# Kernel optimization log

Measured on AMD Instinct MI355X. Metric: run time of the kernel, lower is better.

Reference implementation:

```python
import jax, jax.numpy as jnp
import numpy as np

EMB = 768
HEADS = 12


def setup_inputs() -> dict:
    key = jax.random.key(0)
    ks = jax.random.split(key, 5)
    B, N, E = 8, 1024, EMB
    x = jax.random.normal(ks[0], (B, N, E), dtype=jnp.float32)
    s = 1.0 / np.sqrt(E)
    W_qkv = jax.random.normal(ks[1], (E, 3 * E), dtype=jnp.float32) * s
    b_qkv = jnp.zeros((3 * E,), dtype=jnp.float32)
    W_fc = jax.random.normal(ks[2], (E, E), dtype=jnp.float32) * s
    b_fc = jnp.zeros((E,), dtype=jnp.float32)
    return {"x": x, "W_qkv": W_qkv, "b_qkv": b_qkv, "W_fc": W_fc, "b_fc": b_fc}


def reference(x, W_qkv, b_qkv, W_fc, b_fc):
    B, N, E = x.shape
    H = HEADS
    D = E // H
    qkv = x @ W_qkv + b_qkv                      # [B, N, 3E]
    q, k, v = jnp.split(qkv, 3, axis=-1)
    # b n (h d) -> b h n d
    def to_heads(t):
        return t.reshape(B, N, H, D).transpose(0, 2, 1, 3)
    q, k, v = to_heads(q), to_heads(k), to_heads(v)
    scale = 1.0 / jnp.sqrt(jnp.float32(E))       # NOTE: scales by sqrt(emb_size), not head dim
    attn = jnp.einsum('bhid,bhjd->bhij', q, k) * scale
    attn = jax.nn.softmax(attn, axis=-1)
    out = jnp.einsum('bhij,bhjd->bhid', attn, v)
    out = out.transpose(0, 2, 1, 3).reshape(B, N, E)  # b h n d -> b n (h d)
    return out @ W_fc + b_fc
```

## Files before the change

kernel.cpp:

```cpp
#include <hip/hip_runtime.h>


typedef unsigned short u16;
typedef unsigned int u32;
typedef __attribute__((ext_vector_type(8))) short short8;
typedef __attribute__((ext_vector_type(4))) float f32x4;

#define DEV static __device__ __forceinline__

DEV u16 f2bf(float f) {
  union { float f; u32 u; } v; v.f = f;
  return (u16)((v.u + 0x7FFFu + ((v.u >> 16) & 1u)) >> 16);
}

DEV void gload_lds16(const void* g, void* l) {
  __builtin_amdgcn_global_load_lds(
      (const __attribute__((address_space(1))) void*)g,
      (__attribute__((address_space(3))) void*)l, 16, 0, 0);
}

__global__ void cvt_bf16_kernel(const float* __restrict__ in, u16* __restrict__ out, int n8) {
  int idx = blockIdx.x * blockDim.x + threadIdx.x;
  int stride = gridDim.x * blockDim.x;
  for (int i = idx; i < n8; i += stride) {
    float4 a = reinterpret_cast<const float4*>(in)[2 * i];
    float4 b = reinterpret_cast<const float4*>(in)[2 * i + 1];
    uint4 o;
    o.x = f2bf(a.x) | ((u32)f2bf(a.y) << 16);
    o.y = f2bf(a.z) | ((u32)f2bf(a.w) << 16);
    o.z = f2bf(b.x) | ((u32)f2bf(b.y) << 16);
    o.w = f2bf(b.z) | ((u32)f2bf(b.w) << 16);
    reinterpret_cast<uint4*>(out)[i] = o;
  }
}

__global__ void trcvt_kernel(const float* __restrict__ in, u16* __restrict__ out,
                             int K, int Nn) {
  __shared__ u16 tile[64][72];
  int ntiles = Nn >> 6;
  int tk = blockIdx.x / ntiles, tn = blockIdx.x % ntiles;
  int k0 = tk << 6, n0 = tn << 6;
  int t = threadIdx.x;
  int r = t >> 4;
  int c4 = (t & 15) << 2;
#pragma unroll
  for (int ps = 0; ps < 4; ++ps) {
    int k = r + ps * 16;
    float4 v = *reinterpret_cast<const float4*>(&in[(size_t)(k0 + k) * Nn + n0 + c4]);
    tile[c4 + 0][k] = f2bf(v.x);
    tile[c4 + 1][k] = f2bf(v.y);
    tile[c4 + 2][k] = f2bf(v.z);
    tile[c4 + 3][k] = f2bf(v.w);
  }
  __syncthreads();
  int nr = t >> 3;
  int c8 = (t & 7) << 3;
#pragma unroll
  for (int ps = 0; ps < 2; ++ps) {
    int n = nr + ps * 32;
    uint4 v = *reinterpret_cast<const uint4*>(&tile[n][c8]);
    *reinterpret_cast<uint4*>(&out[(size_t)(n0 + n) * K + k0 + c8]) = v;
  }
}

__global__ void trv_kernel(const u16* __restrict__ vh, u16* __restrict__ vt) {
  __shared__ u16 tile[64][72];
  int nt = blockIdx.x & 15;
  int bh = blockIdx.x >> 4;
  int n0 = nt << 6;
  int t = threadIdx.x;
  int nr = t >> 3;
  int d8 = (t & 7) << 3;
  const u16* src = vh + ((size_t)bh * 1024 + n0) * 64;
#pragma unroll
  for (int ps = 0; ps < 2; ++ps) {
    int n = nr + ps * 32;
    uint4 v = *reinterpret_cast<const uint4*>(&src[(size_t)n * 64 + d8]);
    const u16* e = reinterpret_cast<const u16*>(&v);
#pragma unroll
    for (int j = 0; j < 8; ++j) tile[d8 + j][n] = e[j];
  }
  __syncthreads();
  u16* dst = vt + ((size_t)bh * 64) * 1024 + n0;
#pragma unroll
  for (int ps = 0; ps < 2; ++ps) {
    int d = nr + ps * 32;
    uint4 v = *reinterpret_cast<const uint4*>(&tile[d][d8]);
    *reinterpret_cast<uint4*>(&dst[(size_t)d * 1024 + d8]) = v;
  }
}

template <int MODE>
__global__ __launch_bounds__(256, 4) void gemm_bt(
    const u16* __restrict__ A, const u16* __restrict__ Bt,
    const float* __restrict__ bias, void* __restrict__ Cout,
    u16* __restrict__ qh, u16* __restrict__ kh, u16* __restrict__ vh,
    int Nn) {
  __shared__ u16 As[2][128 * 32];
  __shared__ u16 Bs[2][128 * 32];
  const int nTn = Nn >> 7;
  const int nwg = gridDim.x;
  int wg = blockIdx.x;
  wg = (wg & 7) * (nwg >> 3) + (wg >> 3);
  const int tm = wg / nTn, tn = wg % nTn;
  const int m0 = tm << 7, n0 = tn << 7;
  const int tid = threadIdx.x;
  const int w = tid >> 6, lane = tid & 63;
  const int g = lane >> 4, p = lane & 15;
  const int wr = w >> 1, wc = w & 1;

  const int srow = lane >> 2;
  const int schunk = (lane & 3) ^ ((srow >> 1) & 3);
  const u16* Asrc = A + (size_t)(m0 + srow) * 768 + schunk * 8;
  const u16* Bsrc = Bt + (size_t)(n0 + srow) * 768 + schunk * 8;
  const int csw = (g ^ ((p >> 1) & 3)) << 3;

  f32x4 acc[4][4] = {};

#define STAGE(kt, sbuf)                                                         \
  do {                                                                          \
    _Pragma("unroll")                                                           \
    for (int i = 0; i < 2; ++i) {                                               \
      int trow = w * 32 + i * 16;                                               \
      gload_lds16(Asrc + (size_t)trow * 768 + (kt) * 32, &As[sbuf][trow * 32]); \
      gload_lds16(Bsrc + (size_t)trow * 768 + (kt) * 32, &Bs[sbuf][trow * 32]); \
    }                                                                           \
  } while (0)

  STAGE(0, 0);
  __syncthreads();

  int buf = 0;
  for (int k = 0; k < 24; ++k) {
    const u16* as = As[buf];
    const u16* bs = Bs[buf];
    short8 af[4], bf[4];
#pragma unroll
    for (int mb = 0; mb < 4; ++mb)
      af[mb] = *reinterpret_cast<const short8*>(&as[(wr * 64 + mb * 16 + p) * 32 + csw]);
#pragma unroll
    for (int nb = 0; nb < 4; ++nb)
      bf[nb] = *reinterpret_cast<const short8*>(&bs[(wc * 64 + nb * 16 + p) * 32 + csw]);
    if (k < 23) STAGE(k + 1, buf ^ 1);
#pragma unroll
    for (int mb = 0; mb < 4; ++mb)
#pragma unroll
      for (int nb = 0; nb < 4; ++nb)
        acc[mb][nb] = __builtin_amdgcn_mfma_f32_16x16x32_bf16(af[mb], bf[nb], acc[mb][nb], 0, 0, 0);
    __syncthreads();
    buf ^= 1;
  }
#undef STAGE

  const float qscale = 0.036084391824351615f;
#pragma unroll
  for (int nb = 0; nb < 4; ++nb) {
    int ncol = n0 + wc * 64 + nb * 16 + p;
    float bv = bias[ncol];
    if (MODE == 0) {
#pragma unroll
      for (int mb = 0; mb < 4; ++mb)
#pragma unroll
        for (int r = 0; r < 4; ++r) {
          int m = m0 + wr * 64 + mb * 16 + g * 4 + r;
          ((float*)Cout)[(size_t)m * Nn + ncol] = acc[mb][nb][r] + bv;
        }
    } else {
      int h64 = ncol >> 6;
      int which = h64 / 12;
      int hh = h64 - which * 12;
      int d = ncol & 63;
      u16* dst = which == 0 ? qh : (which == 1 ? kh : vh);
      float sc = which == 0 ? qscale : 1.f;
#pragma unroll
      for (int mb = 0; mb < 4; ++mb)
#pragma unroll
        for (int r = 0; r < 4; ++r) {
          int m = m0 + wr * 64 + mb * 16 + g * 4 + r;
          int bb = m >> 10, nr = m & 1023;
          dst[(((size_t)bb * 12 + hh) * 1024 + nr) * 64 + d] = f2bf((acc[mb][nb][r] + bv) * sc);
        }
    }
  }
}

__global__ __launch_bounds__(512, 6) void attn_kernel(
    const u16* __restrict__ qh, const u16* __restrict__ kh,
    const u16* __restrict__ vt, u16* __restrict__ ao) {
  __shared__ u16 Ks[2][64 * 64];
  __shared__ u16 Vs[2][64 * 64];
  __shared__ u16 Ps[8][16 * 64];
  const int bid = blockIdx.x;
  const int qt = bid & 7;
  const int bh = bid >> 3;
  const int b = bh / 12, h = bh % 12;
  const int tid = threadIdx.x;
  const int w = tid >> 6, lane = tid & 63;
  const int g = lane >> 4, p = lane & 15;
  const int qrow = qt * 128 + w * 16;

  const u16* qbase = qh + ((size_t)bh * 1024 + qrow + p) * 64;
  short8 qf0 = *reinterpret_cast<const short8*>(qbase + g * 8);
  short8 qf1 = *reinterpret_cast<const short8*>(qbase + 32 + g * 8);

  const int ci = w * 64 + lane;
  const int crow = ci >> 3;
  const int csw = (ci & 7) ^ (crow & 7);
  const u16* ksrc = kh + (((size_t)bh * 1024 + crow) << 6) + csw * 8;
  const u16* vsrc = vt + ((size_t)bh * 64 + crow) * 1024 + csw * 8;
  u16* myp = Ps[w];

  const int sw = p & 7;
  const int c0 = (g ^ sw) << 3;
  const int c1 = ((4 + g) ^ sw) << 3;

  float m_run = -1e30f, l_run = 0.f;
  f32x4 oacc[4] = {};

  gload_lds16(ksrc, &Ks[0][w * 512]);
  gload_lds16(vsrc, &Vs[0][w * 512]);
  __syncthreads();

  int buf = 0;
  for (int kt = 0; kt < 1024; kt += 64) {
    if (kt < 960) {
      gload_lds16(ksrc + ((kt + 64) << 6), &Ks[buf ^ 1][w * 512]);
      gload_lds16(vsrc + (kt + 64), &Vs[buf ^ 1][w * 512]);
    }

    f32x4 s[4];
    __builtin_amdgcn_s_setprio(1);
#pragma unroll
    for (int jb = 0; jb < 4; ++jb) {
      const u16* kb = &Ks[buf][(jb * 16 + p) * 64];
      short8 k0 = *reinterpret_cast<const short8*>(kb + c0);
      short8 k1 = *reinterpret_cast<const short8*>(kb + c1);
      f32x4 z = {};
      z = __builtin_amdgcn_mfma_f32_16x16x32_bf16(k0, qf0, z, 0, 0, 0);
      z = __builtin_amdgcn_mfma_f32_16x16x32_bf16(k1, qf1, z, 0, 0, 0);
      s[jb] = z;
    }
    __builtin_amdgcn_s_setprio(0);

    float tmax = -1e30f;
#pragma unroll
    for (int jb = 0; jb < 4; ++jb)
#pragma unroll
      for (int r = 0; r < 4; ++r) tmax = fmaxf(tmax, s[jb][r]);
    tmax = fmaxf(tmax, __shfl_xor(tmax, 16));
    tmax = fmaxf(tmax, __shfl_xor(tmax, 32));
    float m_new = fmaxf(m_run, tmax);
    float alpha = __expf(m_run - m_new);
    float lsum = 0.f;
#pragma unroll
    for (int jb = 0; jb < 4; ++jb)
#pragma unroll
      for (int r = 0; r < 4; ++r) {
        float e = __expf(s[jb][r] - m_new);
        s[jb][r] = e;
        lsum += e;
      }
    lsum += __shfl_xor(lsum, 16);
    lsum += __shfl_xor(lsum, 32);
    l_run = l_run * alpha + lsum;
    m_run = m_new;

#pragma unroll
    for (int jb = 0; jb < 4; ++jb) {
      uint2 pk;
      pk.x = f2bf(s[jb][0]) | ((u32)f2bf(s[jb][1]) << 16);
      pk.y = f2bf(s[jb][2]) | ((u32)f2bf(s[jb][3]) << 16);
      int c = 2 * jb + (g >> 1);
      *reinterpret_cast<uint2*>(&myp[p * 64 + ((c ^ sw) << 3) + ((g & 1) << 2)]) = pk;
    }

    float al[4];
#pragma unroll
    for (int r = 0; r < 4; ++r) al[r] = __shfl(alpha, g * 4 + r);
#pragma unroll
    for (int nb = 0; nb < 4; ++nb)
#pragma unroll
      for (int r = 0; r < 4; ++r) oacc[nb][r] *= al[r];

    short8 pa0 = *reinterpret_cast<const short8*>(&myp[p * 64 + c0]);
    short8 pa1 = *reinterpret_cast<const short8*>(&myp[p * 64 + c1]);
    __builtin_amdgcn_s_setprio(1);
#pragma unroll
    for (int nb = 0; nb < 4; ++nb) {
      const u16* vb = &Vs[buf][(nb * 16 + p) * 64];
      short8 v0 = *reinterpret_cast<const short8*>(vb + c0);
      short8 v1 = *reinterpret_cast<const short8*>(vb + c1);
      oacc[nb] = __builtin_amdgcn_mfma_f32_16x16x32_bf16(pa0, v0, oacc[nb], 0, 0, 0);
      oacc[nb] = __builtin_amdgcn_mfma_f32_16x16x32_bf16(pa1, v1, oacc[nb], 0, 0, 0);
    }
    __builtin_amdgcn_s_setprio(0);

    __syncthreads();
    buf ^= 1;
  }

  float li[4];
#pragma unroll
  for (int r = 0; r < 4; ++r) li[r] = 1.f / __shfl(l_run, g * 4 + r);
  u16* obase = ao + ((size_t)(b * 1024 + qrow)) * 768 + h * 64;
#pragma unroll
  for (int nb = 0; nb < 4; ++nb)
#pragma unroll
    for (int r = 0; r < 4; ++r)
      obase[(size_t)(g * 4 + r) * 768 + nb * 16 + p] = f2bf(oacc[nb][r] * li[r]);
}

extern "C" void kernel_launch(void* const* d_in, const int* in_sizes, int n_in,
                              void* d_out, int out_size, void* d_ws, size_t ws_size,
                              hipStream_t stream) {
  const float* x = (const float*)d_in[0];
  const float* Wqkv = (const float*)d_in[1];
  const float* bqkv = (const float*)d_in[2];
  const float* Wfc = (const float*)d_in[3];
  const float* bfc = (const float*)d_in[4];
  float* out = (float*)d_out;

  char* ws = (char*)d_ws;
  u16* xb    = (u16*)(ws);
  u16* wqkvT = (u16*)(ws + 12582912);
  u16* wfcT  = (u16*)(ws + 16121856);
  u16* qh    = (u16*)(ws + 17301504);
  u16* kh    = (u16*)(ws + 29884416);
  u16* vh    = (u16*)(ws + 42467328);
  u16* vt    = (u16*)(ws + 55050240);
  u16* ao    = (u16*)(ws + 67633152);

  cvt_bf16_kernel<<<2048, 256, 0, stream>>>(x, xb, (8192 * 768) / 8);
  trcvt_kernel<<<12 * 36, 256, 0, stream>>>(Wqkv, wqkvT, 768, 2304);
  trcvt_kernel<<<12 * 12, 256, 0, stream>>>(Wfc, wfcT, 768, 768);
  gemm_bt<2><<<64 * 18, 256, 0, stream>>>(xb, wqkvT, bqkv, nullptr, qh, kh, vh, 2304);
  trv_kernel<<<96 * 16, 256, 0, stream>>>(vh, vt);
  attn_kernel<<<96 * 8, 512, 0, stream>>>(qh, kh, vt, ao);
  gemm_bt<0><<<64 * 6, 256, 0, stream>>>(ao, wfcT, bfc, out, nullptr, nullptr, nullptr, 768);
}
```

Baseline: 140.1 us.

## Replace QKV GEMM with 256x256 8-wave ping-pong kernel writing V transposed

The QKV projection moves to a new 512-thread kernel with 256x256 tiles, K-step 64, double-buffered LDS loaded via global_load_lds, phased barriers and s_setprio to interleave MFMA with loads. The epilogue writes V directly in transposed layout, which removes the separate trv_kernel launch and its extra pass through memory. The cost is a grid of only 288 workgroups (fewer than two waves across the CUs), higher LDS use, and strided 2-byte stores for the V transpose.

After: 165.5 us. +18.1%, slower.

```diff
diff --git a/kernel.cpp b/kernel.cpp
--- a/kernel.cpp
+++ b/kernel.cpp
@@ -63,39 +63,157 @@
   }
 }
 
-__global__ void trv_kernel(const u16* __restrict__ vh, u16* __restrict__ vt) {
-  __shared__ u16 tile[64][72];
-  int nt = blockIdx.x & 15;
-  int bh = blockIdx.x >> 4;
-  int n0 = nt << 6;
-  int t = threadIdx.x;
-  int nr = t >> 3;
-  int d8 = (t & 7) << 3;
-  const u16* src = vh + ((size_t)bh * 1024 + n0) * 64;
-#pragma unroll
-  for (int ps = 0; ps < 2; ++ps) {
-    int n = nr + ps * 32;
-    uint4 v = *reinterpret_cast<const uint4*>(&src[(size_t)n * 64 + d8]);
-    const u16* e = reinterpret_cast<const u16*>(&v);
-#pragma unroll
-    for (int j = 0; j < 8; ++j) tile[d8 + j][n] = e[j];
-  }
-  __syncthreads();
-  u16* dst = vt + ((size_t)bh * 64) * 1024 + n0;
-#pragma unroll
-  for (int ps = 0; ps < 2; ++ps) {
-    int d = nr + ps * 32;
-    uint4 v = *reinterpret_cast<const uint4*>(&tile[d][d8]);
-    *reinterpret_cast<uint4*>(&dst[(size_t)d * 1024 + d8]) = v;
-  }
-}
-
-template <int MODE>
-__global__ __launch_bounds__(256, 4) void gemm_bt(
+__global__ __launch_bounds__(512, 2) void gemm8p_qkv(
     const u16* __restrict__ A, const u16* __restrict__ Bt,
-    const float* __restrict__ bias, void* __restrict__ Cout,
-    u16* __restrict__ qh, u16* __restrict__ kh, u16* __restrict__ vh,
-    int Nn) {
+    const float* __restrict__ bias,
+    u16* __restrict__ qh, u16* __restrict__ kh, u16* __restrict__ vt) {
+  __shared__ u16 As[2][256 * 64];
+  __shared__ u16 Bs[2][256 * 64];
+  int wg = blockIdx.x;
+  wg = (wg & 7) * 36 + (wg >> 3);
+  const int tm = wg / 9, tn = wg % 9;
+  const int m0 = tm << 8, n0 = tn << 8;
+  const int tid = threadIdx.x;
+  const int w = tid >> 6, lane = tid & 63;
+  const int g = lane >> 4, p = lane & 15;
+  const int wr = w >> 2, wc = w & 3;
+
+  const int srow8 = lane >> 3;
+  const int sch = (lane & 7) ^ srow8;
+  const u16* Abase = A + (size_t)(m0 + w * 8 + srow8) * 768 + sch * 8;
+  const u16* Bbase = Bt + (size_t)(n0 + w * 8 + srow8) * 768 + sch * 8;
+  const int c0 = (g ^ (p & 7)) << 3;
+  const int c1 = ((4 + g) ^ (p & 7)) << 3;
+
+  u16* A0 = As[0]; u16* A1 = As[1];
+  u16* B0 = Bs[0]; u16* B1 = Bs[1];
+
+  f32x4 acc[8][4] = {};
+  short8 af[4][2], bf[4][2];
+
+#define STG(Xbase, XS, half, tile)                                             \
+  do {                                                                         \
+    gload_lds16(Xbase + (size_t)((half) * 128) * 768 + (size_t)(tile) * 64,    \
+                &XS[((half) * 128 + w * 8) * 64]);                             \
+    gload_lds16(Xbase + (size_t)((half) * 128 + 64) * 768 + (size_t)(tile) * 64, \
+                &XS[((half) * 128 + 64 + w * 8) * 64]);                        \
+  } while (0)
+
+#define RDA(XS, moff)                                                          \
+  do {                                                                         \
+    _Pragma("unroll") for (int mb = 0; mb < 4; ++mb) {                         \
+      const u16* ra = &XS[(wr * 128 + (moff) + mb * 16 + p) * 64];             \
+      af[mb][0] = *reinterpret_cast<const short8*>(ra + c0);                   \
+      af[mb][1] = *reinterpret_cast<const short8*>(ra + c1);                   \
+    }                                                                          \
+  } while (0)
+
+#define RDB(XS, nb0)                                                           \
+  do {                                                                         \
+    _Pragma("unroll") for (int nn = 0; nn < 2; ++nn) {                         \
+      const u16* rb = &XS[(wc * 64 + ((nb0) + nn) * 16 + p) * 64];             \
+      bf[(nb0) + nn][0] = *reinterpret_cast<const short8*>(rb + c0);           \
+      bf[(nb0) + nn][1] = *reinterpret_cast<const short8*>(rb + c1);           \
+    }                                                                          \
+  } while (0)
+
+#define MM(mo, no)                                                             \
+  do {                                                                         \
+    _Pragma("unroll") for (int mb = 0; mb < 4; ++mb)                           \
+    _Pragma("unroll") for (int nn = 0; nn < 2; ++nn) {                         \
+      acc[(mo) + mb][(no) + nn] = __builtin_amdgcn_mfma_f32_16x16x32_bf16(     \
+          af[mb][0], bf[(no) + nn][0], acc[(mo) + mb][(no) + nn], 0, 0, 0);    \
+      acc[(mo) + mb][(no) + nn] = __builtin_amdgcn_mfma_f32_16x16x32_bf16(     \
+          af[mb][1], bf[(no) + nn][1], acc[(mo) + mb][(no) + nn], 0, 0, 0);    \
+    }                                                                          \
+  } while (0)
+
+#define PH_SYNC                                                                \
+  __builtin_amdgcn_s_barrier();                                                \
+  asm volatile("s_waitcnt lgkmcnt(0)" ::: "memory");                           \
+  __builtin_amdgcn_s_setprio(1);
+
+#define PH_END                                                                 \
+  __builtin_amdgcn_s_setprio(0);                                               \
+  __builtin_amdgcn_s_barrier();
+
+  STG(Abase, A0, 0, 0); STG(Abase, A0, 1, 0);
+  STG(Bbase, B0, 0, 0); STG(Bbase, B0, 1, 0);
+  STG(Bbase, B1, 0, 1); STG(Bbase, B1, 1, 1);
+  STG(Abase, A1, 0, 1);
+  asm volatile("s_waitcnt vmcnt(6)" ::: "memory");
+  __builtin_amdgcn_s_barrier();
+
+#pragma unroll 1
+  for (int t = 0; t < 6; ++t) {
+    const int T1 = 2 * t + 1, T2 = 2 * t + 2, T3 = 2 * t + 3;
+    const bool more = (t < 5);
+    RDA(A0, 0); RDB(B0, 0);
+    STG(Abase, A1, 1, T1);
+    PH_SYNC; MM(0, 0); PH_END;
+    RDB(B0, 2);
+    PH_SYNC; MM(0, 2); PH_END;
+    RDA(A0, 64);
+    if (more) STG(Bbase, B0, 0, T2);
+    PH_SYNC; MM(4, 0); PH_END;
+    if (more) STG(Bbase, B0, 1, T2);
+    PH_SYNC; MM(4, 2);
+    __builtin_amdgcn_s_setprio(0);
+    if (more) asm volatile("s_waitcnt vmcnt(4)" ::: "memory");
+    else      asm volatile("s_waitcnt vmcnt(0)" ::: "memory");
+    __builtin_amdgcn_s_barrier();
+    RDA(A1, 0); RDB(B1, 0);
+    if (more) STG(Abase, A0, 0, T2);
+    PH_SYNC; MM(0, 0); PH_END;
+    RDB(B1, 2);
+    if (more) STG(Abase, A0, 1, T2);
+    PH_SYNC; MM(0, 2); PH_END;
+    RDA(A1, 64);
+    if (more) STG(Bbase, B1, 0, T3);
+    PH_SYNC; MM(4, 0); PH_END;
+    if (more) { STG(Bbase, B1, 1, T3); STG(Abase, A1, 0, T3); }
+    PH_SYNC; MM(4, 2);
+    __builtin_amdgcn_s_setprio(0);
+    if (more) asm volatile("s_waitcnt vmcnt(6)" ::: "memory");
+    __builtin_amdgcn_s_barrier();
+  }
+#undef STG
+#undef RDA
+#undef RDB
+#undef MM
+#undef PH_SYNC
+#undef PH_END
+
+  const float qscale = 0.036084391824351615f;
+#pragma unroll
+  for (int nb = 0; nb < 4; ++nb) {
+    int ncol = n0 + wc * 64 + nb * 16 + p;
+    float bv = bias[ncol];
+    int h64 = ncol >> 6;
+    int which = h64 / 12;
+    int hh = h64 - which * 12;
+    int d = ncol & 63;
+#pragma unroll
+    for (int mb = 0; mb < 8; ++mb)
+#pragma unroll
+      for (int r = 0; r < 4; ++r) {
+        int m = m0 + wr * 128 + mb * 16 + g * 4 + r;
+        int bb = m >> 10, nr = m & 1023;
+        float vv = acc[mb][nb][r] + bv;
+        if (which == 2) {
+          vt[((size_t)(bb * 12 + hh) * 64 + d) * 1024 + nr] = f2bf(vv);
+        } else {
+          u16* dst = which == 0 ? qh : kh;
+          float sc = which == 0 ? qscale : 1.f;
+          dst[(((size_t)bb * 12 + hh) * 1024 + nr) * 64 + d] = f2bf(vv * sc);
+        }
+      }
+  }
+}
+
+__global__ __launch_bounds__(256, 4) void gemm_bt_f32(
+    const u16* __restrict__ A, const u16* __restrict__ Bt,
+    const float* __restrict__ bias, float* __restrict__ Cout, int Nn) {
   __shared__ u16 As[2][128 * 32];
   __shared__ u16 Bs[2][128 * 32];
   const int nTn = Nn >> 7;
@@ -152,35 +270,17 @@
   }
 #undef STAGE
 
-  const float qscale = 0.036084391824351615f;
 #pragma unroll
   for (int nb = 0; nb < 4; ++nb) {
     int ncol = n0 + wc * 64 + nb * 16 + p;
     float bv = bias[ncol];
-    if (MODE == 0) {
-#pragma unroll
-      for (int mb = 0; mb < 4; ++mb)
-#pragma unroll
-        for (int r = 0; r < 4; ++r) {
-          int m = m0 + wr * 64 + mb * 16 + g * 4 + r;
-          ((float*)Cout)[(size_t)m * Nn + ncol] = acc[mb][nb][r] + bv;
-        }
-    } else {
-      int h64 = ncol >> 6;
-      int which = h64 / 12;
-      int hh = h64 - which * 12;
-      int d = ncol & 63;
-      u16* dst = which == 0 ? qh : (which == 1 ? kh : vh);
-      float sc = which == 0 ? qscale : 1.f;
-#pragma unroll
-      for (int mb = 0; mb < 4; ++mb)
-#pragma unroll
-        for (int r = 0; r < 4; ++r) {
-          int m = m0 + wr * 64 + mb * 16 + g * 4 + r;
-          int bb = m >> 10, nr = m & 1023;
-          dst[(((size_t)bb * 12 + hh) * 1024 + nr) * 64 + d] = f2bf((acc[mb][nb][r] + bv) * sc);
-        }
-    }
+#pragma unroll
+    for (int mb = 0; mb < 4; ++mb)
+#pragma unroll
+      for (int r = 0; r < 4; ++r) {
+        int m = m0 + wr * 64 + mb * 16 + g * 4 + r;
+        Cout[(size_t)m * Nn + ncol] = acc[mb][nb][r] + bv;
+      }
   }
 }
 
@@ -326,15 +426,13 @@
   u16* wfcT  = (u16*)(ws + 16121856);
   u16* qh    = (u16*)(ws + 17301504);
   u16* kh    = (u16*)(ws + 29884416);
-  u16* vh    = (u16*)(ws + 42467328);
   u16* vt    = (u16*)(ws + 55050240);
   u16* ao    = (u16*)(ws + 67633152);
 
   cvt_bf16_kernel<<<2048, 256, 0, stream>>>(x, xb, (8192 * 768) / 8);
   trcvt_kernel<<<12 * 36, 256, 0, stream>>>(Wqkv, wqkvT, 768, 2304);
   trcvt_kernel<<<12 * 12, 256, 0, stream>>>(Wfc, wfcT, 768, 768);
-  gemm_bt<2><<<64 * 18, 256, 0, stream>>>(xb, wqkvT, bqkv, nullptr, qh, kh, vh, 2304);
-  trv_kernel<<<96 * 16, 256, 0, stream>>>(vh, vt);
+  gemm8p_qkv<<<288, 512, 0, stream>>>(xb, wqkvT, bqkv, qh, kh, vt);
   attn_kernel<<<96 * 8, 512, 0, stream>>>(qh, kh, vt, ao);
-  gemm_bt<0><<<64 * 6, 256, 0, stream>>>(ao, wfcT, bfc, out, nullptr, nullptr, nullptr, 768);
-}
+  gemm_bt_f32<<<64 * 6, 256, 0, stream>>>(ao, wfcT, bfc, out, 768);
+}
```

## Fuse V transpose into QKV epilogue and use lazy exp2 softmax rescaling

Applied to the files above, without the earlier changes.

The QKV GEMM epilogue now writes V directly in transposed [b,h,d,n] layout, which removes the separate trv_kernel launch and its extra read/write pass over V. The Q scale is folded with log2(e) so the attention softmax can use the native exp2 instruction. The running-max rescale of the output accumulator is skipped unless the new tile max exceeds the running max by more than 8, which trades some fp32 headroom for fewer multiplies. P packing now uses the hip bf16 conversion intrinsics. The transposed V stores in the GEMM epilogue are strided rather than coalesced, which could slow that epilogue.

After: 142.7 us. Within noise of the previous version (+1.9%).

```diff
diff --git a/kernel.cpp b/kernel.cpp
--- a/kernel.cpp
+++ b/kernel.cpp
@@ -1,4 +1,5 @@
 #include <hip/hip_runtime.h>
+#include <hip/hip_bf16.h>
 
 
 typedef unsigned short u16;
@@ -11,6 +12,13 @@
 DEV u16 f2bf(float f) {
   union { float f; u32 u; } v; v.f = f;
   return (u16)((v.u + 0x7FFFu + ((v.u >> 16) & 1u)) >> 16);
+}
+
+DEV u32 pk2(float lo, float hi) {
+  union { __hip_bfloat162 h2; u32 u; } v;
+  v.h2.x = __float2bfloat16(lo);
+  v.h2.y = __float2bfloat16(hi);
+  return v.u;
 }
 
 DEV void gload_lds16(const void* g, void* l) {
@@ -63,38 +71,11 @@
   }
 }
 
-__global__ void trv_kernel(const u16* __restrict__ vh, u16* __restrict__ vt) {
-  __shared__ u16 tile[64][72];
-  int nt = blockIdx.x & 15;
-  int bh = blockIdx.x >> 4;
-  int n0 = nt << 6;
-  int t = threadIdx.x;
-  int nr = t >> 3;
-  int d8 = (t & 7) << 3;
-  const u16* src = vh + ((size_t)bh * 1024 + n0) * 64;
-#pragma unroll
-  for (int ps = 0; ps < 2; ++ps) {
-    int n = nr + ps * 32;
-    uint4 v = *reinterpret_cast<const uint4*>(&src[(size_t)n * 64 + d8]);
-    const u16* e = reinterpret_cast<const u16*>(&v);
-#pragma unroll
-    for (int j = 0; j < 8; ++j) tile[d8 + j][n] = e[j];
-  }
-  __syncthreads();
-  u16* dst = vt + ((size_t)bh * 64) * 1024 + n0;
-#pragma unroll
-  for (int ps = 0; ps < 2; ++ps) {
-    int d = nr + ps * 32;
-    uint4 v = *reinterpret_cast<const uint4*>(&tile[d][d8]);
-    *reinterpret_cast<uint4*>(&dst[(size_t)d * 1024 + d8]) = v;
-  }
-}
-
 template <int MODE>
 __global__ __launch_bounds__(256, 4) void gemm_bt(
     const u16* __restrict__ A, const u16* __restrict__ Bt,
     const float* __restrict__ bias, void* __restrict__ Cout,
-    u16* __restrict__ qh, u16* __restrict__ kh, u16* __restrict__ vh,
+    u16* __restrict__ qh, u16* __restrict__ kh, u16* __restrict__ vt,
     int Nn) {
   __shared__ u16 As[2][128 * 32];
   __shared__ u16 Bs[2][128 * 32];
@@ -152,7 +133,7 @@
   }
 #undef STAGE
 
-  const float qscale = 0.036084391824351615f;
+  const float qscale = 0.05205878290161879f;
 #pragma unroll
   for (int nb = 0; nb < 4; ++nb) {
     int ncol = n0 + wc * 64 + nb * 16 + p;
@@ -170,15 +151,20 @@
       int which = h64 / 12;
       int hh = h64 - which * 12;
       int d = ncol & 63;
-      u16* dst = which == 0 ? qh : (which == 1 ? kh : vh);
-      float sc = which == 0 ? qscale : 1.f;
 #pragma unroll
       for (int mb = 0; mb < 4; ++mb)
 #pragma unroll
         for (int r = 0; r < 4; ++r) {
           int m = m0 + wr * 64 + mb * 16 + g * 4 + r;
           int bb = m >> 10, nr = m & 1023;
-          dst[(((size_t)bb * 12 + hh) * 1024 + nr) * 64 + d] = f2bf((acc[mb][nb][r] + bv) * sc);
+          float vv = acc[mb][nb][r] + bv;
+          if (which == 2) {
+            vt[((size_t)(bb * 12 + hh) * 64 + d) * 1024 + nr] = f2bf(vv);
+          } else {
+            u16* dst = which == 0 ? qh : kh;
+            float sc = which == 0 ? qscale : 1.f;
+            dst[(((size_t)bb * 12 + hh) * 1024 + nr) * 64 + d] = f2bf(vv * sc);
+          }
         }
     }
   }
@@ -249,38 +235,42 @@
       for (int r = 0; r < 4; ++r) tmax = fmaxf(tmax, s[jb][r]);
     tmax = fmaxf(tmax, __shfl_xor(tmax, 16));
     tmax = fmaxf(tmax, __shfl_xor(tmax, 32));
-    float m_new = fmaxf(m_run, tmax);
-    float alpha = __expf(m_run - m_new);
+
+    if (!__all(tmax - m_run <= 8.f)) {
+      float m_new = fmaxf(m_run, tmax);
+      float alpha = __builtin_amdgcn_exp2f(m_run - m_new);
+      float al[4];
+#pragma unroll
+      for (int r = 0; r < 4; ++r) al[r] = __shfl(alpha, g * 4 + r);
+#pragma unroll
+      for (int nb = 0; nb < 4; ++nb)
+#pragma unroll
+        for (int r = 0; r < 4; ++r) oacc[nb][r] *= al[r];
+      l_run *= alpha;
+      m_run = m_new;
+    }
+
     float lsum = 0.f;
 #pragma unroll
     for (int jb = 0; jb < 4; ++jb)
 #pragma unroll
       for (int r = 0; r < 4; ++r) {
-        float e = __expf(s[jb][r] - m_new);
+        float e = __builtin_amdgcn_exp2f(s[jb][r] - m_run);
         s[jb][r] = e;
         lsum += e;
       }
     lsum += __shfl_xor(lsum, 16);
     lsum += __shfl_xor(lsum, 32);
-    l_run = l_run * alpha + lsum;
-    m_run = m_new;
+    l_run += lsum;
 
 #pragma unroll
     for (int jb = 0; jb < 4; ++jb) {
-      uint2 pk;
-      pk.x = f2bf(s[jb][0]) | ((u32)f2bf(s[jb][1]) << 16);
-      pk.y = f2bf(s[jb][2]) | ((u32)f2bf(s[jb][3]) << 16);
+      uint2 pkv;
+      pkv.x = pk2(s[jb][0], s[jb][1]);
+      pkv.y = pk2(s[jb][2], s[jb][3]);
       int c = 2 * jb + (g >> 1);
-      *reinterpret_cast<uint2*>(&myp[p * 64 + ((c ^ sw) << 3) + ((g & 1) << 2)]) = pk;
-    }
-
-    float al[4];
-#pragma unroll
-    for (int r = 0; r < 4; ++r) al[r] = __shfl(alpha, g * 4 + r);
-#pragma unroll
-    for (int nb = 0; nb < 4; ++nb)
-#pragma unroll
-      for (int r = 0; r < 4; ++r) oacc[nb][r] *= al[r];
+      *reinterpret_cast<uint2*>(&myp[p * 64 + ((c ^ sw) << 3) + ((g & 1) << 2)]) = pkv;
+    }
 
     short8 pa0 = *reinterpret_cast<const short8*>(&myp[p * 64 + c0]);
     short8 pa1 = *reinterpret_cast<const short8*>(&myp[p * 64 + c1]);
@@ -326,15 +316,13 @@
   u16* wfcT  = (u16*)(ws + 16121856);
   u16* qh    = (u16*)(ws + 17301504);
   u16* kh    = (u16*)(ws + 29884416);
-  u16* vh    = (u16*)(ws + 42467328);
   u16* vt    = (u16*)(ws + 55050240);
   u16* ao    = (u16*)(ws + 67633152);
 
   cvt_bf16_kernel<<<2048, 256, 0, stream>>>(x, xb, (8192 * 768) / 8);
   trcvt_kernel<<<12 * 36, 256, 0, stream>>>(Wqkv, wqkvT, 768, 2304);
   trcvt_kernel<<<12 * 12, 256, 0, stream>>>(Wfc, wfcT, 768, 768);
-  gemm_bt<2><<<64 * 18, 256, 0, stream>>>(xb, wqkvT, bqkv, nullptr, qh, kh, vh, 2304);
-  trv_kernel<<<96 * 16, 256, 0, stream>>>(vh, vt);
+  gemm_bt<2><<<64 * 18, 256, 0, stream>>>(xb, wqkvT, bqkv, nullptr, qh, kh, vt, 2304);
   attn_kernel<<<96 * 8, 512, 0, stream>>>(qh, kh, vt, ao);
   gemm_bt<0><<<64 * 6, 256, 0, stream>>>(ao, wfcT, bfc, out, nullptr, nullptr, nullptr, 768);
 }
```
